# Kernel tuning notes

Measured on AMD Instinct MI355X. Metric: run time of the kernel, lower is better.

Reference implementation:

```python
import jax, jax.numpy as jnp
import numpy as np


def hadamard_transform(x):
    """Normalized fast Walsh-Hadamard transform along the last axis.

    Equivalent to x @ H_n / sqrt(n) with H_n the Sylvester Hadamard matrix.
    Last dim must be a power of two. Computed in fp32 (rotate_fp32=True).
    """
    orig_dtype = x.dtype
    x = x.astype(jnp.float32)
    n = x.shape[-1]
    lead = x.shape[:-1]
    x = x.reshape(-1, n)  # (B, n)
    h = 1
    while h < n:
        # butterfly stage: pairs separated by h
        x = x.reshape(-1, n // (2 * h), 2, h)
        a = x[:, :, 0, :]
        b = x[:, :, 1, :]
        x = jnp.stack([a + b, a - b], axis=2).reshape(-1, n)
        h *= 2
    x = x * (1.0 / np.sqrt(n)).astype(np.float32)
    return x.reshape(lead + (n,)).astype(orig_dtype)


def setup_inputs() -> dict:
    key = jax.random.key(0)
    k1, k2, k3 = jax.random.split(key, 3)
    B, S, D_IN, D_OUT = 4, 2048, 8192, 2048
    x = jax.random.normal(k1, (B, S, D_IN), dtype=jnp.float32)
    # nn.Linear params: weight (out, in), bias (out,) with kaiming-ish scale
    W = jax.random.normal(k2, (D_OUT, D_IN), dtype=jnp.float32) * (1.0 / np.sqrt(D_IN))
    b = jax.random.normal(k3, (D_OUT,), dtype=jnp.float32) * 0.01
    return {"x": x, "W": W, "b": b}


def reference(x, W, b):
    xh = hadamard_transform(x)                      # (B, S, D_in)
    return jnp.einsum('bsd,od->bso', xh, W) + b     # (B, S, D_out)
```

## Files before the change

kernel.cpp:

```cpp
#include <hip/hip_runtime.h>
#include <hip/hip_bf16.h>
#include <stdint.h>


#define M_TOTAL 8192
#define K_TOTAL 8192
#define N_TOTAL 2048
#define D_IN 8192

typedef __attribute__((ext_vector_type(8))) short short8;
typedef __attribute__((ext_vector_type(4))) float f32x4;

typedef __attribute__((address_space(1))) void void_g;
typedef __attribute__((address_space(3))) void void_l;
typedef __attribute__((address_space(3))) short lds_s3;

__device__ __forceinline__ short f2bf(float f) {
  __hip_bfloat16 h = __float2bfloat16(f);
  return *reinterpret_cast<short*>(&h);
}

__global__ void cvt_x_kernel(const float* __restrict__ x, short* __restrict__ xb, long n) {
  long stride = (long)gridDim.x * blockDim.x * 8;
  for (long i = ((long)blockIdx.x * blockDim.x + threadIdx.x) * 8; i < n; i += stride) {
    float4 v0 = *(const float4*)(x + i);
    float4 v1 = *(const float4*)(x + i + 4);
    short8 o;
    o[0] = f2bf(v0.x); o[1] = f2bf(v0.y); o[2] = f2bf(v0.z); o[3] = f2bf(v0.w);
    o[4] = f2bf(v1.x); o[5] = f2bf(v1.y); o[6] = f2bf(v1.z); o[7] = f2bf(v1.w);
    *(short8*)(xb + i) = o;
  }
}

__global__ void fwht_w_kernel(const float* __restrict__ W, short* __restrict__ Wh) {
  __shared__ float buf[D_IN];
  const int row = blockIdx.x;
  const float* src = W + (long)row * D_IN;
  for (int i = threadIdx.x; i < D_IN / 4; i += blockDim.x)
    ((float4*)buf)[i] = ((const float4*)src)[i];
  for (int h = 1; h < D_IN; h <<= 1) {
    __syncthreads();
    for (int p = threadIdx.x; p < D_IN / 2; p += blockDim.x) {
      int i = ((p & ~(h - 1)) << 1) | (p & (h - 1));
      float a = buf[i], b = buf[i + h];
      buf[i] = a + b;
      buf[i + h] = a - b;
    }
  }
  __syncthreads();
  const float s = 0.011048543456039806f;
  short* dst = Wh + (long)row * D_IN;
  for (int i = threadIdx.x; i < D_IN; i += blockDim.x)
    dst[i] = f2bf(buf[i] * s);
}

#define NT 128

#define ADST(D, H) (((D) * 2 + (H)) * 8192 + sdst)
#define BDST(D, H) (32768 + ((D) * 2 + (H)) * 8192 + sdst)

#define STG(DST, SRC, KOFF)                                                                       \
  __builtin_amdgcn_global_load_lds((void_g*)((SRC) + (KOFF)), (void_l*)&lds[DST], 16, 0, 0);      \
  __builtin_amdgcn_global_load_lds((void_g*)((SRC) + (KOFF) + 64 * (long)K_TOTAL),                \
                                   (void_l*)&lds[(DST) + 4096], 16, 0, 0);

#define DSR(dst, ADDR, IMM)                                                                       \
  asm volatile("ds_read_b128 %0, %1 offset:%2" : "=v"(dst) : "v"(ADDR), "i"(IMM))

#define RD_A4(D, MIB)                                                                             \
  DSR(am[0][0], aAd0, (D) * 32768 + ((MIB) + 0) * 2048);                                          \
  DSR(am[0][1], aAd1, (D) * 32768 + ((MIB) + 0) * 2048);                                          \
  DSR(am[1][0], aAd0, (D) * 32768 + ((MIB) + 1) * 2048);                                          \
  DSR(am[1][1], aAd1, (D) * 32768 + ((MIB) + 1) * 2048);                                          \
  DSR(am[2][0], aAd0, (D) * 32768 + ((MIB) + 2) * 2048);                                          \
  DSR(am[2][1], aAd1, (D) * 32768 + ((MIB) + 2) * 2048);                                          \
  DSR(am[3][0], aAd0, (D) * 32768 + ((MIB) + 3) * 2048);                                          \
  DSR(am[3][1], aAd1, (D) * 32768 + ((MIB) + 3) * 2048);

#define RD_B2(D, NJB)                                                                             \
  DSR(bn[(NJB) + 0][0], bAd0, (D) * 32768 + ((NJB) + 0) * 2048);                                  \
  DSR(bn[(NJB) + 0][1], bAd1, (D) * 32768 + ((NJB) + 0) * 2048);                                  \
  DSR(bn[(NJB) + 1][0], bAd0, (D) * 32768 + ((NJB) + 1) * 2048);                                  \
  DSR(bn[(NJB) + 1][1], bAd1, (D) * 32768 + ((NJB) + 1) * 2048);

#define MF(MIB, NJB)                                                                              \
  __builtin_amdgcn_s_setprio(1);                                                                  \
  _Pragma("unroll") for (int mi = 0; mi < 4; ++mi) {                                              \
    _Pragma("unroll") for (int nj = 0; nj < 2; ++nj) {                                            \
      _Pragma("unroll") for (int ks = 0; ks < 2; ++ks) acc[(MIB) + mi][(NJB) + nj] =              \
          __builtin_amdgcn_mfma_f32_16x16x32_bf16(am[mi][ks], bn[(NJB) + nj][ks],                 \
                                                  acc[(MIB) + mi][(NJB) + nj], 0, 0, 0);          \
    }                                                                                             \
  }                                                                                               \
  __builtin_amdgcn_s_setprio(0);

#define BAR __builtin_amdgcn_s_barrier()
#define SBAR __builtin_amdgcn_sched_barrier(0)
#define LG0 do { asm volatile("s_waitcnt lgkmcnt(0)"); SBAR; } while (0)

#define KTILE(D, STGA, KA, STGB, KB, FN, DOF, LB)                                                 \
  {                                                                                               \
                                                                        \
    RD_B2(D, 0);                                                                                  \
    RD_A4(D, 0);                                                                                  \
    if (STGA) { STG(ADST(D ^ 1, 0), aSrc0, KA); }                                                 \
    asm volatile("s_waitcnt lgkmcnt(8)");                                                         \
    BAR;                                                                                          \
    LG0;                                                                                          \
    MF(0, 0);                                                                                     \
    BAR;                                                                                          \
                                                                        \
    RD_B2(D, 2);                                                                                  \
    if (STGA) { STG(ADST(D ^ 1, 1), aSrc1, KA); }                                                 \
    BAR;                                                                                          \
    LG0;                                                                                          \
    MF(0, 2);                                                                                     \
    BAR;                                                                                          \
                                                                        \
    RD_A4(D, 4);                                                                                  \
    if (STGB) { STG(BDST(D, 0), bSrc0, KB); }                                                     \
    BAR;                                                                                          \
    LG0;                                                                                          \
    MF(4, 0);                                                                                     \
    BAR;                                                                                          \
                                                                 \
    if (STGB) { STG(BDST(D, 1), bSrc1, KB); }                                                     \
    BAR;                                                                                          \
    MF(4, 2);                                                                                     \
    if (DOF) { asm volatile("s_waitcnt vmcnt(" FN ")"); }                                         \
    if (LB) BAR;                                                                                  \
  }

__global__ __launch_bounds__(512, 2) void gemm_kernel(const short* __restrict__ A,
                                                      const short* __restrict__ B,
                                                      const float* __restrict__ bias,
                                                      float* __restrict__ C) {
  __shared__ __attribute__((aligned(16))) short lds[65536];

  const int tid = threadIdx.x;
  const int l = tid & 63;
  const int w = tid >> 6;
  const int wm = w >> 2;
  const int wn = w & 3;
  const int wh = wn >> 1;

  const int bid = blockIdx.x;
  const int swz = (bid & 7) * 32 + (bid >> 3);
  const int bm = swz >> 3;
  const int bn_ = swz & 7;
  const long tileM = (long)bm * 256;
  const long tileN = (long)bn_ * 256;

  const int slot0 = (l >> 4) ^ (l & 7);
  const int laneb = (l & 15) * 128 + slot0 * 16;
  const unsigned ldsb = (unsigned)(uintptr_t)(lds_s3*)&lds[0];
  const unsigned aAd0 = ldsb + (unsigned)(wm * 16384 + laneb);
  const unsigned aAd1 = aAd0 ^ 64u;
  const unsigned bAd0 = ldsb + 65536u + (unsigned)(wh * 16384 + (wn & 1) * 8192 + laneb);
  const unsigned bAd1 = bAd0 ^ 64u;

  const int sdst = tid * 8;
  const int srow = tid >> 3;
  const int sslot = ((tid & 7) ^ (srow & 7)) * 8;
  const short* aSrc0 = A + (tileM + srow) * (long)K_TOTAL + sslot;
  const short* aSrc1 = aSrc0 + 128 * (long)K_TOTAL;
  const short* bSrc0 = B + (tileN + srow) * (long)K_TOTAL + sslot;
  const short* bSrc1 = bSrc0 + 128 * (long)K_TOTAL;

  f32x4 acc[8][4];
#pragma unroll
  for (int mi = 0; mi < 8; ++mi)
#pragma unroll
    for (int nj = 0; nj < 4; ++nj)
      acc[mi][nj] = (f32x4){0.f, 0.f, 0.f, 0.f};

  STG(ADST(0, 0), aSrc0, 0);
  STG(ADST(0, 1), aSrc1, 0);
  STG(BDST(0, 0), bSrc0, 0);
  STG(BDST(0, 1), bSrc1, 0);
  STG(BDST(1, 0), bSrc0, 64);
  STG(BDST(1, 1), bSrc1, 64);
  asm volatile("s_waitcnt vmcnt(4)");
  BAR;

  short8 am[4][2], bn[4][2];

  for (int t = 0; t < NT - 2; t += 2) {
    KTILE(0, true, (t + 1) * 64, true, (t + 2) * 64, "4", true, true);
    KTILE(1, true, (t + 2) * 64, true, (t + 3) * 64, "4", true, true);
  }
  KTILE(0, true, 127 * 64, false, 0, "0", true, true);
  KTILE(1, false, 0, false, 0, "0", false, false);

  const int rb = (int)tileM + wm * 128 + (l >> 4) * 4;
  const int cb = (int)tileN + wn * 64 + (l & 15);
#pragma unroll
  for (int mi = 0; mi < 8; ++mi)
#pragma unroll
    for (int nj = 0; nj < 4; ++nj) {
      float bv = bias[cb + nj * 16];
      const int r0 = rb + mi * 16;
#pragma unroll
      for (int r = 0; r < 4; ++r)
        C[(long)(r0 + r) * N_TOTAL + cb + nj * 16] = acc[mi][nj][r] + bv;
    }
}

extern "C" void kernel_launch(void* const* d_in, const int* in_sizes, int n_in,
                              void* d_out, int out_size, void* d_ws, size_t ws_size,
                              hipStream_t stream) {
  const float* x = (const float*)d_in[0];
  const float* W = (const float*)d_in[1];
  const float* bias = (const float*)d_in[2];
  float* out = (float*)d_out;

  short* xb = (short*)d_ws;
  short* wh = (short*)((char*)d_ws + (size_t)M_TOTAL * K_TOTAL * 2);

  cvt_x_kernel<<<2048, 256, 0, stream>>>(x, xb, (long)M_TOTAL * K_TOTAL);
  fwht_w_kernel<<<N_TOTAL, 256, 0, stream>>>(W, wh);

  const int grid = (M_TOTAL / 256) * (N_TOTAL / 256);
  gemm_kernel<<<grid, 512, 0, stream>>>(xb, wh, bias, out);
}
```

Baseline: 336.5 us.

## Fuse fp32-to-bf16 conversion of x into GEMM A-tile loading

Drops the separate cvt_x kernel. The GEMM now loads fp32 x tiles straight into registers, converts them to bf16 and writes them to LDS with ds_write. This removes a full read-write pass over the 64M-element bf16 copy of x. The cost is that the A operand now moves through registers instead of direct global-to-LDS loads, and each GEMM tile reads twice the bytes from fp32 (x is re-read by the 8 N-tile blocks). The vmcnt waits are replaced with lgkmcnt waits.

```diff
diff --git a/kernel.cpp b/kernel.cpp
--- a/kernel.cpp
+++ b/kernel.cpp
@@ -20,16 +20,11 @@
   return *reinterpret_cast<short*>(&h);
 }
 
-__global__ void cvt_x_kernel(const float* __restrict__ x, short* __restrict__ xb, long n) {
-  long stride = (long)gridDim.x * blockDim.x * 8;
-  for (long i = ((long)blockIdx.x * blockDim.x + threadIdx.x) * 8; i < n; i += stride) {
-    float4 v0 = *(const float4*)(x + i);
-    float4 v1 = *(const float4*)(x + i + 4);
-    short8 o;
-    o[0] = f2bf(v0.x); o[1] = f2bf(v0.y); o[2] = f2bf(v0.z); o[3] = f2bf(v0.w);
-    o[4] = f2bf(v1.x); o[5] = f2bf(v1.y); o[6] = f2bf(v1.z); o[7] = f2bf(v1.w);
-    *(short8*)(xb + i) = o;
-  }
+__device__ __forceinline__ short8 cvt8(float4 a, float4 b) {
+  short8 s;
+  s[0] = f2bf(a.x); s[1] = f2bf(a.y); s[2] = f2bf(a.z); s[3] = f2bf(a.w);
+  s[4] = f2bf(b.x); s[5] = f2bf(b.y); s[6] = f2bf(b.z); s[7] = f2bf(b.w);
+  return s;
 }
 
 __global__ void fwht_w_kernel(const float* __restrict__ W, short* __restrict__ Wh) {
@@ -56,7 +51,6 @@
 
 #define NT 128
 
-#define ADST(D, H) (((D) * 2 + (H)) * 8192 + sdst)
 #define BDST(D, H) (32768 + ((D) * 2 + (H)) * 8192 + sdst)
 
 #define STG(DST, SRC, KOFF)                                                                       \
@@ -66,6 +60,12 @@
 
 #define DSR(dst, ADDR, IMM)                                                                       \
   asm volatile("ds_read_b128 %0, %1 offset:%2" : "=v"(dst) : "v"(ADDR), "i"(IMM))
+
+#define AWR(D, H, SA, SB)                                                                         \
+  asm volatile("ds_write_b128 %0, %1 offset:%2" ::"v"(awA), "v"(SA),                              \
+               "i"(((D) * 2 + (H)) * 16384) : "memory");                                          \
+  asm volatile("ds_write_b128 %0, %1 offset:%2" ::"v"(awA), "v"(SB),                              \
+               "i"(((D) * 2 + (H)) * 16384 + 8192) : "memory");
 
 #define RD_A4(D, MIB)                                                                             \
   DSR(am[0][0], aAd0, (D) * 32768 + ((MIB) + 0) * 2048);                                          \
@@ -98,40 +98,48 @@
 #define SBAR __builtin_amdgcn_sched_barrier(0)
 #define LG0 do { asm volatile("s_waitcnt lgkmcnt(0)"); SBAR; } while (0)
 
-#define KTILE(D, STGA, KA, STGB, KB, FN, DOF, LB)                                                 \
+#define KTILE(D, STGA, KA, STGB, KB, LB)                                                          \
   {                                                                                               \
-                                                                        \
     RD_B2(D, 0);                                                                                  \
     RD_A4(D, 0);                                                                                  \
-    if (STGA) { STG(ADST(D ^ 1, 0), aSrc0, KA); }                                                 \
+    if (STGA) {                                                                                   \
+      a00 = *(const float4*)(aF0 + (KA));                                                         \
+      a01 = *(const float4*)(aF0 + (KA) + 4);                                                     \
+      a02 = *(const float4*)(aF1 + (KA));                                                         \
+      a03 = *(const float4*)(aF1 + (KA) + 4);                                                     \
+    }                                                                                             \
     asm volatile("s_waitcnt lgkmcnt(8)");                                                         \
     BAR;                                                                                          \
     LG0;                                                                                          \
     MF(0, 0);                                                                                     \
     BAR;                                                                                          \
-                                                                        \
     RD_B2(D, 2);                                                                                  \
-    if (STGA) { STG(ADST(D ^ 1, 1), aSrc1, KA); }                                                 \
+    if (STGA) {                                                                                   \
+      a10 = *(const float4*)(aF2 + (KA));                                                         \
+      a11 = *(const float4*)(aF2 + (KA) + 4);                                                     \
+      a12 = *(const float4*)(aF3 + (KA));                                                         \
+      a13 = *(const float4*)(aF3 + (KA) + 4);                                                     \
+    }                                                                                             \
     BAR;                                                                                          \
     LG0;                                                                                          \
     MF(0, 2);                                                                                     \
     BAR;                                                                                          \
-                                                                        \
     RD_A4(D, 4);                                                                                  \
+    if (STGA) { AWR(D ^ 1, 0, cvt8(a00, a01), cvt8(a02, a03)); }                                  \
     if (STGB) { STG(BDST(D, 0), bSrc0, KB); }                                                     \
     BAR;                                                                                          \
     LG0;                                                                                          \
     MF(4, 0);                                                                                     \
     BAR;                                                                                          \
-                                                                 \
+    if (STGA) { AWR(D ^ 1, 1, cvt8(a10, a11), cvt8(a12, a13)); }                                  \
     if (STGB) { STG(BDST(D, 1), bSrc1, KB); }                                                     \
     BAR;                                                                                          \
     MF(4, 2);                                                                                     \
-    if (DOF) { asm volatile("s_waitcnt vmcnt(" FN ")"); }                                         \
+    asm volatile("s_waitcnt lgkmcnt(0)");                                                         \
     if (LB) BAR;                                                                                  \
   }
 
-__global__ __launch_bounds__(512, 2) void gemm_kernel(const short* __restrict__ A,
+__global__ __launch_bounds__(512, 2) void gemm_kernel(const float* __restrict__ X,
                                                       const short* __restrict__ B,
                                                       const float* __restrict__ bias,
                                                       float* __restrict__ C) {
@@ -161,11 +169,14 @@
 
   const int sdst = tid * 8;
   const int srow = tid >> 3;
-  const int sslot = ((tid & 7) ^ (srow & 7)) * 8;
-  const short* aSrc0 = A + (tileM + srow) * (long)K_TOTAL + sslot;
-  const short* aSrc1 = aSrc0 + 128 * (long)K_TOTAL;
-  const short* bSrc0 = B + (tileN + srow) * (long)K_TOTAL + sslot;
+  const int scol = ((tid & 7) ^ (srow & 7)) * 8;
+  const float* aF0 = X + (tileM + srow) * (long)K_TOTAL + scol;
+  const float* aF1 = aF0 + 64 * (long)K_TOTAL;
+  const float* aF2 = aF0 + 128 * (long)K_TOTAL;
+  const float* aF3 = aF0 + 192 * (long)K_TOTAL;
+  const short* bSrc0 = B + (tileN + srow) * (long)K_TOTAL + scol;
   const short* bSrc1 = bSrc0 + 128 * (long)K_TOTAL;
+  const unsigned awA = ldsb + (unsigned)tid * 16u;
 
   f32x4 acc[8][4];
 #pragma unroll
@@ -174,23 +185,34 @@
     for (int nj = 0; nj < 4; ++nj)
       acc[mi][nj] = (f32x4){0.f, 0.f, 0.f, 0.f};
 
-  STG(ADST(0, 0), aSrc0, 0);
-  STG(ADST(0, 1), aSrc1, 0);
+  float4 a00, a01, a02, a03, a10, a11, a12, a13;
+
+  a00 = *(const float4*)(aF0);
+  a01 = *(const float4*)(aF0 + 4);
+  a02 = *(const float4*)(aF1);
+  a03 = *(const float4*)(aF1 + 4);
+  a10 = *(const float4*)(aF2);
+  a11 = *(const float4*)(aF2 + 4);
+  a12 = *(const float4*)(aF3);
+  a13 = *(const float4*)(aF3 + 4);
   STG(BDST(0, 0), bSrc0, 0);
   STG(BDST(0, 1), bSrc1, 0);
   STG(BDST(1, 0), bSrc0, 64);
   STG(BDST(1, 1), bSrc1, 64);
-  asm volatile("s_waitcnt vmcnt(4)");
+  AWR(0, 0, cvt8(a00, a01), cvt8(a02, a03));
+  AWR(0, 1, cvt8(a10, a11), cvt8(a12, a13));
+  asm volatile("s_waitcnt vmcnt(0)");
+  asm volatile("s_waitcnt lgkmcnt(0)");
   BAR;
 
   short8 am[4][2], bn[4][2];
 
   for (int t = 0; t < NT - 2; t += 2) {
-    KTILE(0, true, (t + 1) * 64, true, (t + 2) * 64, "4", true, true);
-    KTILE(1, true, (t + 2) * 64, true, (t + 3) * 64, "4", true, true);
+    KTILE(0, true, (t + 1) * 64, true, (t + 2) * 64, true);
+    KTILE(1, true, (t + 2) * 64, true, (t + 3) * 64, true);
   }
-  KTILE(0, true, 127 * 64, false, 0, "0", true, true);
-  KTILE(1, false, 0, false, 0, "0", false, false);
+  KTILE(0, true, 127 * 64, false, 0, true);
+  KTILE(1, false, 0, false, 0, false);
 
   const int rb = (int)tileM + wm * 128 + (l >> 4) * 4;
   const int cb = (int)tileN + wn * 64 + (l & 15);
@@ -214,12 +236,10 @@
   const float* bias = (const float*)d_in[2];
   float* out = (float*)d_out;
 
-  short* xb = (short*)d_ws;
-  short* wh = (short*)((char*)d_ws + (size_t)M_TOTAL * K_TOTAL * 2);
-
-  cvt_x_kernel<<<2048, 256, 0, stream>>>(x, xb, (long)M_TOTAL * K_TOTAL);
+  short* wh = (short*)d_ws;
+
   fwht_w_kernel<<<N_TOTAL, 256, 0, stream>>>(W, wh);
 
   const int grid = (M_TOTAL / 256) * (N_TOTAL / 256);
-  gemm_kernel<<<grid, 512, 0, stream>>>(xb, wh, bias, out);
-}
+  gemm_kernel<<<grid, 512, 0, stream>>>(x, wh, bias, out);
+}
```

After: 447.8 us. 33.1% more time.
